# Kernel optimization log

Measured on AMD Instinct MI355X. Metric: run time of the kernel, lower is better.

Reference implementation:

```python
import jax, jax.numpy as jnp
import numpy as np

ACT_BIT = 8
W_BIT = 8
EPS = 1e-8


def ste_round(x):
    # straight-through round (matches torch STE quant autograd)
    return x + jax.lax.stop_gradient(jnp.round(x) - x)


def quant_act(x):
    """Per-tensor symmetric 8-bit activation quantization (HAWQ QuantAct)."""
    n = 2 ** (ACT_BIT - 1) - 1  # 127
    x_max = jax.lax.stop_gradient(jnp.max(jnp.abs(x)))
    scale = jnp.maximum(x_max, EPS) / n
    x_int = jnp.clip(ste_round(x / scale), -n - 1, n)
    return x_int * scale, scale


def quant_linear(x_q, act_scale, weight, bias):
    """Per-channel symmetric 8-bit weight quant + integer matmul + fused dequant."""
    n = 2 ** (W_BIT - 1) - 1  # 127
    w_max = jax.lax.stop_gradient(jnp.max(jnp.abs(weight), axis=1, keepdims=True))  # [out,1]
    w_scale = jnp.maximum(w_max, EPS) / n                                            # [out,1]
    w_int = jnp.clip(ste_round(weight / w_scale), -n - 1, n)                         # [out,in]
    bias_scale = w_scale[:, 0] * act_scale                                           # [out]
    b_int = ste_round(bias / bias_scale)                                             # [out]
    x_int = x_q / act_scale                                   # integer-valued float, [..., in]
    out_int = jnp.einsum('...i,oi->...o', x_int, w_int)       # int8-domain GEMM in float
    return (out_int + b_int) * bias_scale                     # fused dequant


def setup_inputs() -> dict:
    key = jax.random.key(0)
    k1, k2, k3 = jax.random.split(key, 3)
    L, B, Q, D, O = 6, 8, 1024, 1024, 1024
    hs = jax.random.normal(k1, (L, B, Q, D), dtype=jnp.float32)
    weight = jax.random.normal(k2, (O, D), dtype=jnp.float32) * 0.02
    bias = jax.random.normal(k3, (O,), dtype=jnp.float32) * 0.02
    return {"hs": hs, "weight": weight, "bias": bias}


def reference(hs, weight, bias):
    x_q, act_scale = quant_act(hs)
    return quant_linear(x_q, act_scale, weight, bias)
```

## Files before the change

### kernel.cpp

```cpp
#include <hip/hip_runtime.h>
#include <stdint.h>

typedef int i32x4 __attribute__((ext_vector_type(4)));

#define K_DIM 1024
#define BM 128
#define BN 256
#define BKK 64

__device__ __forceinline__ int quant1(float v, float inv) {
  float t = rintf(v * inv);
  t = fminf(fmaxf(t, -128.0f), 127.0f);
  return (int)t;
}

__device__ __forceinline__ void gld_lds16(const signed char* g, signed char* l) {
  typedef const __attribute__((address_space(1))) unsigned int* gp_t;
  typedef __attribute__((address_space(3))) unsigned int* lp_t;
  __builtin_amdgcn_global_load_lds((gp_t)(const void*)g, (lp_t)(void*)l, 16, 0, 0);
}

__global__ void absmax_kernel(const float* __restrict__ x, unsigned int* __restrict__ amax,
                              long long n4) {
  long long i = (long long)blockIdx.x * blockDim.x + threadIdx.x;
  const long long stride = (long long)gridDim.x * blockDim.x;
  const float4* x4 = (const float4*)x;
  float m = 0.0f;
  for (; i < n4; i += stride) {
    float4 v = x4[i];
    m = fmaxf(m, fmaxf(fmaxf(fabsf(v.x), fabsf(v.y)), fmaxf(fabsf(v.z), fabsf(v.w))));
  }
#pragma unroll
  for (int off = 32; off > 0; off >>= 1) m = fmaxf(m, __shfl_down(m, off, 64));
  __shared__ float sm[4];
  const int lane = threadIdx.x & 63, wid = threadIdx.x >> 6;
  if (lane == 0) sm[wid] = m;
  __syncthreads();
  if (threadIdx.x == 0) {
    float b = fmaxf(fmaxf(sm[0], sm[1]), fmaxf(sm[2], sm[3]));
    atomicMax(amax, __float_as_uint(b));
  }
}

__global__ void wquant_kernel(const float* __restrict__ w, const float* __restrict__ bias,
                              const unsigned int* __restrict__ amax_u,
                              signed char* __restrict__ wq,
                              float* __restrict__ bscale, float* __restrict__ bint) {
  const int o = blockIdx.x;
  const int t = threadIdx.x;
  float4 v = ((const float4*)(w + (size_t)o * K_DIM))[t];
  float m = fmaxf(fmaxf(fabsf(v.x), fabsf(v.y)), fmaxf(fabsf(v.z), fabsf(v.w)));
#pragma unroll
  for (int off = 32; off > 0; off >>= 1) m = fmaxf(m, __shfl_down(m, off, 64));
  __shared__ float sm[4];
  __shared__ float s_scale;
  const int lane = t & 63, wid = t >> 6;
  if (lane == 0) sm[wid] = m;
  __syncthreads();
  if (t == 0) {
    float wm = fmaxf(fmaxf(sm[0], sm[1]), fmaxf(sm[2], sm[3]));
    float wsc = fmaxf(wm, 1e-8f) / 127.0f;
    float asc = fmaxf(__uint_as_float(*amax_u), 1e-8f) / 127.0f;
    float bsc = wsc * asc;
    bscale[o] = bsc;
    bint[o] = rintf(bias[o] / bsc);
    s_scale = wsc;
  }
  __syncthreads();
  const float inv = 1.0f / s_scale;
  int q0 = quant1(v.x, inv), q1 = quant1(v.y, inv), q2 = quant1(v.z, inv), q3 = quant1(v.w, inv);
  unsigned int p = (unsigned)(q0 & 255) | ((unsigned)(q1 & 255) << 8) |
                   ((unsigned)(q2 & 255) << 16) | ((unsigned)(q3 & 255) << 24);
  ((unsigned int*)wq)[o * 256 + t] = p;
}

__global__ void aquant_kernel(const float* __restrict__ x, const unsigned int* __restrict__ amax_u,
                              unsigned int* __restrict__ q4, long long n4) {
  const float asc = fmaxf(__uint_as_float(*amax_u), 1e-8f) / 127.0f;
  const float inv = 1.0f / asc;
  long long i = (long long)blockIdx.x * blockDim.x + threadIdx.x;
  const long long stride = (long long)gridDim.x * blockDim.x;
  const float4* x4 = (const float4*)x;
  for (; i < n4; i += stride) {
    float4 v = x4[i];
    int q0 = quant1(v.x, inv), q1 = quant1(v.y, inv), q2 = quant1(v.z, inv), q3 = quant1(v.w, inv);
    q4[i] = (unsigned)(q0 & 255) | ((unsigned)(q1 & 255) << 8) |
            ((unsigned)(q2 & 255) << 16) | ((unsigned)(q3 & 255) << 24);
  }
}

__global__ __launch_bounds__(256, 2) void gemm_kernel(
    const signed char* __restrict__ A, const signed char* __restrict__ W,
    const float* __restrict__ bscale, const float* __restrict__ bint,
    float* __restrict__ out, int M, int N, int K) {
  __shared__ __align__(16) signed char Alds[2][8][1024];
  __shared__ __align__(16) signed char Blds[2][16][1024];

  const int nwg = gridDim.x;
  const int orig = blockIdx.x;
  const int wgid = (orig & 7) * (nwg >> 3) + (orig >> 3);
  const int nbn = N / BN;
  const int bm = wgid / nbn;
  const int bn = wgid % nbn;
  const int m0 = bm * BM, n0 = bn * BN;

  const int tid = threadIdx.x;
  const int lane = tid & 63;
  const int wid = tid >> 6;
  const int wr = wid >> 1;
  const int wc = wid & 1;

  const int fr = lane & 15;
  const int fk = (lane >> 4) << 4;

  const signed char* ga = A + (size_t)(m0 + wid * 16 + fr) * K + fk;
  const signed char* gb = W + (size_t)(n0 + wid * 16 + fr) * K + fk;
  const size_t rs = (size_t)64 * K;

  i32x4 acc[4][8];
#pragma unroll
  for (int i = 0; i < 4; i++)
#pragma unroll
    for (int j = 0; j < 8; j++) acc[i][j] = (i32x4){0, 0, 0, 0};

#define STAGE(buf, kof)                                         \
  do {                                                          \
    gld_lds16(ga + (kof),          &Alds[buf][wid][0]);         \
    gld_lds16(ga + (kof) + rs,     &Alds[buf][wid + 4][0]);     \
    gld_lds16(gb + (kof),          &Blds[buf][wid][0]);         \
    gld_lds16(gb + (kof) + rs,     &Blds[buf][wid + 4][0]);     \
    gld_lds16(gb + (kof) + 2 * rs, &Blds[buf][wid + 8][0]);     \
    gld_lds16(gb + (kof) + 3 * rs, &Blds[buf][wid + 12][0]);    \
  } while (0)

  STAGE(0, 0);
  asm volatile("s_waitcnt vmcnt(0)" ::: "memory");
  __syncthreads();

  const int nkt = K / BKK;
  int cur = 0;
  for (int kt = 0; kt < nkt; ++kt) {
    if (kt + 1 < nkt) STAGE(cur ^ 1, (kt + 1) * BKK);
    i32x4 af[4], bf[8];
#pragma unroll
    for (int i = 0; i < 4; i++)
      af[i] = *(const i32x4*)&Alds[cur][wr * 4 + i][lane * 16];
#pragma unroll
    for (int j = 0; j < 8; j++)
      bf[j] = *(const i32x4*)&Blds[cur][wc * 8 + j][lane * 16];
#pragma unroll
    for (int i = 0; i < 4; i++)
#pragma unroll
      for (int j = 0; j < 8; j++)
        acc[i][j] = __builtin_amdgcn_mfma_i32_16x16x64_i8(af[i], bf[j], acc[i][j], 0, 0, 0);
    __syncthreads();
    cur ^= 1;
  }
#undef STAGE

  const int crow0 = m0 + wr * 64;
  const int ccol0 = n0 + wc * 128;
  const int rr = (lane >> 4) * 4;
  const int cc = lane & 15;
#pragma unroll
  for (int j = 0; j < 8; j++) {
    const int col = ccol0 + j * 16 + cc;
    const float bs = bscale[col];
    const float bi = bint[col];
#pragma unroll
    for (int i = 0; i < 4; i++) {
      const int row = crow0 + i * 16 + rr;
#pragma unroll
      for (int r = 0; r < 4; r++) {
        out[(size_t)(row + r) * N + col] = ((float)acc[i][j][r] + bi) * bs;
      }
    }
  }
}

extern "C" void kernel_launch(void* const* d_in, const int* in_sizes, int n_in,
                              void* d_out, int out_size, void* d_ws, size_t ws_size,
                              hipStream_t stream) {
  const float* hs = (const float*)d_in[0];
  const float* w = (const float*)d_in[1];
  const float* bias = (const float*)d_in[2];
  float* out = (float*)d_out;

  const long long n = (long long)in_sizes[0];
  const int K = K_DIM;
  const int O = in_sizes[2];
  const int M = (int)(n / K);

  char* ws = (char*)d_ws;
  unsigned int* amax_u = (unsigned int*)ws;
  float* bscale = (float*)(ws + 256);
  float* bint = (float*)(ws + 256 + 4096);
  signed char* wq = (signed char*)(ws + 65536);
  signed char* xq = (signed char*)(ws + 65536 + 1048576);

  hipMemsetAsync(amax_u, 0, 4, stream);

  const long long n4 = n / 4;
  absmax_kernel<<<2048, 256, 0, stream>>>(hs, amax_u, n4);
  wquant_kernel<<<O, 256, 0, stream>>>(w, bias, amax_u, wq, bscale, bint);
  aquant_kernel<<<2048, 256, 0, stream>>>(hs, amax_u, (unsigned int*)xq, n4);

  const int nblocks = (M / BM) * (O / BN);
  gemm_kernel<<<nblocks, 256, 0, stream>>>(xq, wq, bscale, bint, out, M, O, K);
}
```

Before: 213.8 us.

## Triple-buffer GEMM LDS staging with explicit vmcnt waits and nontemporal stores

Moves the int8 GEMM from a double-buffered to a triple-buffered LDS pipeline that prefetches two k-tiles ahead. It uses explicit vmcnt counters and split barriers so loads stay in flight across iterations, and raises wave priority around the MFMA block. Output stores become nontemporal to avoid polluting cache. LDS use grows from 48KB to 72KB per block, which may limit the two-blocks-per-CU occupancy.

```diff
diff --git a/kernel.cpp b/kernel.cpp
--- a/kernel.cpp
+++ b/kernel.cpp
@@ -93,8 +93,8 @@
     const signed char* __restrict__ A, const signed char* __restrict__ W,
     const float* __restrict__ bscale, const float* __restrict__ bint,
     float* __restrict__ out, int M, int N, int K) {
-  __shared__ __align__(16) signed char Alds[2][8][1024];
-  __shared__ __align__(16) signed char Blds[2][16][1024];
+  __shared__ __align__(16) signed char Alds[3][8][1024];
+  __shared__ __align__(16) signed char Blds[3][16][1024];
 
   const int nwg = gridDim.x;
   const int orig = blockIdx.x;
@@ -133,29 +133,46 @@
     gld_lds16(gb + (kof) + 3 * rs, &Blds[buf][wid + 12][0]);    \
   } while (0)
 
+#define BODY(cur, WAITIMM)                                              \
+  do {                                                                  \
+    asm volatile("s_waitcnt vmcnt(" #WAITIMM ")" ::: "memory");         \
+    __builtin_amdgcn_sched_barrier(0);                                  \
+    __builtin_amdgcn_s_barrier();                                       \
+    __builtin_amdgcn_sched_barrier(0);                                  \
+    i32x4 af[4], bf[8];                                                 \
+    _Pragma("unroll")                                                   \
+    for (int i = 0; i < 4; i++)                                         \
+      af[i] = *(const i32x4*)&Alds[cur][wr * 4 + i][lane * 16];         \
+    _Pragma("unroll")                                                   \
+    for (int j = 0; j < 8; j++)                                         \
+      bf[j] = *(const i32x4*)&Blds[cur][wc * 8 + j][lane * 16];         \
+    asm volatile("s_waitcnt lgkmcnt(0)" ::: "memory");                  \
+    __builtin_amdgcn_sched_barrier(0);                                  \
+    __builtin_amdgcn_s_barrier();                                       \
+    __builtin_amdgcn_sched_barrier(0);                                  \
+    __builtin_amdgcn_s_setprio(1);                                      \
+    _Pragma("unroll")                                                   \
+    for (int i = 0; i < 4; i++)                                         \
+      _Pragma("unroll")                                                 \
+      for (int j = 0; j < 8; j++)                                       \
+        acc[i][j] = __builtin_amdgcn_mfma_i32_16x16x64_i8(af[i], bf[j], acc[i][j], 0, 0, 0); \
+    __builtin_amdgcn_s_setprio(0);                                      \
+  } while (0)
+
+  const int nkt = K / BKK;
   STAGE(0, 0);
-  asm volatile("s_waitcnt vmcnt(0)" ::: "memory");
-  __syncthreads();
-
-  const int nkt = K / BKK;
+  STAGE(1, BKK);
   int cur = 0;
-  for (int kt = 0; kt < nkt; ++kt) {
-    if (kt + 1 < nkt) STAGE(cur ^ 1, (kt + 1) * BKK);
-    i32x4 af[4], bf[8];
-#pragma unroll
-    for (int i = 0; i < 4; i++)
-      af[i] = *(const i32x4*)&Alds[cur][wr * 4 + i][lane * 16];
-#pragma unroll
-    for (int j = 0; j < 8; j++)
-      bf[j] = *(const i32x4*)&Blds[cur][wc * 8 + j][lane * 16];
-#pragma unroll
-    for (int i = 0; i < 4; i++)
-#pragma unroll
-      for (int j = 0; j < 8; j++)
-        acc[i][j] = __builtin_amdgcn_mfma_i32_16x16x64_i8(af[i], bf[j], acc[i][j], 0, 0, 0);
-    __syncthreads();
-    cur ^= 1;
-  }
+  for (int kt = 0; kt < nkt - 2; ++kt) {
+    const int nx2 = cur + 2 >= 3 ? cur - 1 : cur + 2;
+    STAGE(nx2, (kt + 2) * BKK);
+    BODY(cur, 12);
+    cur = cur + 1 >= 3 ? 0 : cur + 1;
+  }
+  BODY(cur, 6);
+  cur = cur + 1 >= 3 ? 0 : cur + 1;
+  BODY(cur, 0);
+#undef BODY
 #undef STAGE
 
   const int crow0 = m0 + wr * 64;
@@ -172,7 +189,8 @@
       const int row = crow0 + i * 16 + rr;
 #pragma unroll
       for (int r = 0; r < 4; r++) {
-        out[(size_t)(row + r) * N + col] = ((float)acc[i][j][r] + bi) * bs;
+        __builtin_nontemporal_store(((float)acc[i][j][r] + bi) * bs,
+                                    &out[(size_t)(row + r) * N + col]);
       }
     }
   }
```

Result: faster. 200.3 us (-6.3%).

## Enlarge GEMM tile to 256x256 with 4-stage LDS pipeline and 8 waves

Applied to the files above, without the earlier changes.

Restructures the int8 GEMM to use 256x256 block tiles with 512 threads (8 waves) and a four-buffer ring in 128 KB of dynamic LDS. Tiles are prefetched three steps ahead with direct global-to-LDS loads. The MFMA work is split into four phases that interleave LDS fragment reads with barriers, waitcnt control and raised wave priority. The aim is better reuse per LDS byte and more global-load latency hiding. In exchange, occupancy drops to one block per CU and the extra barriers add synchronisation overhead.

```diff
diff --git a/kernel.cpp b/kernel.cpp
--- a/kernel.cpp
+++ b/kernel.cpp
@@ -4,9 +4,10 @@
 typedef int i32x4 __attribute__((ext_vector_type(4)));
 
 #define K_DIM 1024
-#define BM 128
+#define BM 256
 #define BN 256
 #define BKK 64
+#define NKT (K_DIM / BKK)
 
 __device__ __forceinline__ int quant1(float v, float inv) {
   float t = rintf(v * inv);
@@ -89,12 +90,13 @@
   }
 }
 
-__global__ __launch_bounds__(256, 2) void gemm_kernel(
+__global__ __launch_bounds__(512, 2) void gemm_kernel(
     const signed char* __restrict__ A, const signed char* __restrict__ W,
     const float* __restrict__ bscale, const float* __restrict__ bint,
     float* __restrict__ out, int M, int N, int K) {
-  __shared__ __align__(16) signed char Alds[2][8][1024];
-  __shared__ __align__(16) signed char Blds[2][16][1024];
+  extern __shared__ __align__(16) signed char smem[];
+  signed char* Abase = smem;
+  signed char* Bbase = smem + 65536;
 
   const int nwg = gridDim.x;
   const int orig = blockIdx.x;
@@ -107,68 +109,114 @@
   const int tid = threadIdx.x;
   const int lane = tid & 63;
   const int wid = tid >> 6;
-  const int wr = wid >> 1;
-  const int wc = wid & 1;
+  const int wr = wid >> 2;
+  const int wc = wid & 3;
 
   const int fr = lane & 15;
   const int fk = (lane >> 4) << 4;
 
   const signed char* ga = A + (size_t)(m0 + wid * 16 + fr) * K + fk;
   const signed char* gb = W + (size_t)(n0 + wid * 16 + fr) * K + fk;
-  const size_t rs = (size_t)64 * K;
-
-  i32x4 acc[4][8];
-#pragma unroll
-  for (int i = 0; i < 4; i++)
-#pragma unroll
-    for (int j = 0; j < 8; j++) acc[i][j] = (i32x4){0, 0, 0, 0};
-
-#define STAGE(buf, kof)                                         \
-  do {                                                          \
-    gld_lds16(ga + (kof),          &Alds[buf][wid][0]);         \
-    gld_lds16(ga + (kof) + rs,     &Alds[buf][wid + 4][0]);     \
-    gld_lds16(gb + (kof),          &Blds[buf][wid][0]);         \
-    gld_lds16(gb + (kof) + rs,     &Blds[buf][wid + 4][0]);     \
-    gld_lds16(gb + (kof) + 2 * rs, &Blds[buf][wid + 8][0]);     \
-    gld_lds16(gb + (kof) + 3 * rs, &Blds[buf][wid + 12][0]);    \
+  const size_t rs = (size_t)128 * K;
+
+  i32x4 acc[8][4];
+#pragma unroll
+  for (int i = 0; i < 8; i++)
+#pragma unroll
+    for (int j = 0; j < 4; j++) acc[i][j] = (i32x4){0, 0, 0, 0};
+
+  i32x4 af[4], bf[4];
+
+#define SB __builtin_amdgcn_sched_barrier(0)
+#define BAR __builtin_amdgcn_s_barrier()
+#define WAIT_LGKM0 asm volatile("s_waitcnt lgkmcnt(0)" ::: "memory")
+
+#define ISSUE_TILE(t)                                                     \
+  do {                                                                    \
+    const int b_ = (t) & 3;                                               \
+    const int kof_ = (t) * BKK;                                           \
+    gld_lds16(ga + kof_,      Abase + ((b_ * 16 + wid) << 10));           \
+    gld_lds16(ga + kof_ + rs, Abase + ((b_ * 16 + wid + 8) << 10));       \
+    gld_lds16(gb + kof_,      Bbase + ((b_ * 16 + wid) << 10));           \
+    gld_lds16(gb + kof_ + rs, Bbase + ((b_ * 16 + wid + 8) << 10));       \
   } while (0)
 
-  STAGE(0, 0);
-  asm volatile("s_waitcnt vmcnt(0)" ::: "memory");
-  __syncthreads();
-
-  const int nkt = K / BKK;
-  int cur = 0;
-  for (int kt = 0; kt < nkt; ++kt) {
-    if (kt + 1 < nkt) STAGE(cur ^ 1, (kt + 1) * BKK);
-    i32x4 af[4], bf[8];
-#pragma unroll
-    for (int i = 0; i < 4; i++)
-      af[i] = *(const i32x4*)&Alds[cur][wr * 4 + i][lane * 16];
-#pragma unroll
-    for (int j = 0; j < 8; j++)
-      bf[j] = *(const i32x4*)&Blds[cur][wc * 8 + j][lane * 16];
-#pragma unroll
-    for (int i = 0; i < 4; i++)
-#pragma unroll
-      for (int j = 0; j < 8; j++)
-        acc[i][j] = __builtin_amdgcn_mfma_i32_16x16x64_i8(af[i], bf[j], acc[i][j], 0, 0, 0);
-    __syncthreads();
-    cur ^= 1;
-  }
-#undef STAGE
-
-  const int crow0 = m0 + wr * 64;
-  const int ccol0 = n0 + wc * 128;
+#define RD_A(i_, mf_) af[i_] = *(const i32x4*)(Abase + (((buf_ * 16) + (mf_)) << 10) + lane * 16)
+#define RD_B(j_, nf_) bf[j_] = *(const i32x4*)(Bbase + (((buf_ * 16) + (nf_)) << 10) + lane * 16)
+
+#define MFMA8(IB, JB)                                                          \
+  do {                                                                         \
+    __builtin_amdgcn_s_setprio(1);                                             \
+    _Pragma("unroll") for (int i_ = 0; i_ < 4; i_++)                           \
+      _Pragma("unroll") for (int j_ = 0; j_ < 2; j_++)                         \
+        acc[(IB) + i_][(JB) + j_] = __builtin_amdgcn_mfma_i32_16x16x64_i8(     \
+            af[i_], bf[(JB) + j_], acc[(IB) + i_][(JB) + j_], 0, 0, 0);        \
+    __builtin_amdgcn_s_setprio(0);                                             \
+  } while (0)
+
+#define TILE(t, DO_ISSUE, VMWAIT)                                              \
+  do {                                                                         \
+    const int buf_ = (t) & 3;                                                  \
+                                                                  \
+    RD_A(0, wr * 8 + 0); RD_A(1, wr * 8 + 1);                                  \
+    RD_A(2, wr * 8 + 2); RD_A(3, wr * 8 + 3);                                  \
+    RD_B(0, wc * 4 + 0); RD_B(1, wc * 4 + 1);                                  \
+    if (DO_ISSUE) ISSUE_TILE((t) + 3);                                         \
+    SB; BAR; SB; WAIT_LGKM0; SB;                                               \
+    MFMA8(0, 0);                                                               \
+    SB; BAR;                                                                   \
+                                                                  \
+    RD_B(2, wc * 4 + 2); RD_B(3, wc * 4 + 3);                                  \
+    SB; BAR; SB; WAIT_LGKM0; SB;                                               \
+    MFMA8(0, 2);                                                               \
+    SB; BAR;                                                                   \
+                                                                  \
+    RD_A(0, wr * 8 + 4); RD_A(1, wr * 8 + 5);                                  \
+    RD_A(2, wr * 8 + 6); RD_A(3, wr * 8 + 7);                                  \
+    SB; BAR; SB; WAIT_LGKM0; SB;                                               \
+    MFMA8(4, 2);                                                               \
+    SB; BAR;                                                                   \
+     \
+    asm volatile("s_waitcnt " VMWAIT ::: "memory");                            \
+    SB; BAR; SB;                                                               \
+    MFMA8(4, 0);                                                               \
+    SB; BAR;                                                                   \
+  } while (0)
+
+  ISSUE_TILE(0);
+  ISSUE_TILE(1);
+  ISSUE_TILE(2);
+  asm volatile("s_waitcnt vmcnt(8)" ::: "memory");
+  SB; BAR; SB;
+
+#pragma unroll 1
+  for (int t = 0; t < NKT - 3; ++t) {
+    TILE(t, 1, "vmcnt(8)");
+  }
+  TILE(NKT - 3, 0, "vmcnt(4)");
+  TILE(NKT - 2, 0, "vmcnt(0)");
+  TILE(NKT - 1, 0, "vmcnt(0)");
+
+#undef TILE
+#undef MFMA8
+#undef RD_A
+#undef RD_B
+#undef ISSUE_TILE
+#undef WAIT_LGKM0
+#undef BAR
+#undef SB
+
+  const int crow0 = m0 + wr * 128;
+  const int ccol0 = n0 + wc * 64;
   const int rr = (lane >> 4) * 4;
   const int cc = lane & 15;
 #pragma unroll
-  for (int j = 0; j < 8; j++) {
+  for (int j = 0; j < 4; j++) {
     const int col = ccol0 + j * 16 + cc;
     const float bs = bscale[col];
     const float bi = bint[col];
 #pragma unroll
-    for (int i = 0; i < 4; i++) {
+    for (int i = 0; i < 8; i++) {
       const int row = crow0 + i * 16 + rr;
 #pragma unroll
       for (int r = 0; r < 4; r++) {
@@ -198,6 +246,9 @@
   signed char* wq = (signed char*)(ws + 65536);
   signed char* xq = (signed char*)(ws + 65536 + 1048576);
 
+  hipFuncSetAttribute((const void*)gemm_kernel,
+                      hipFuncAttributeMaxDynamicSharedMemorySize, 131072);
+
   hipMemsetAsync(amax_u, 0, 4, stream);
 
   const long long n4 = n / 4;
@@ -206,5 +257,5 @@
   aquant_kernel<<<2048, 256, 0, stream>>>(hs, amax_u, (unsigned int*)xq, n4);
 
   const int nblocks = (M / BM) * (O / BN);
-  gemm_kernel<<<nblocks, 256, 0, stream>>>(xq, wq, bscale, bint, out, M, O, K);
-}
+  gemm_kernel<<<nblocks, 512, 131072, stream>>>(xq, wq, bscale, bint, out, M, O, K);
+}
```

After: 216.5 us. About the same (+1.3%).
